# Kernel tuning notes

Hardware: AMD Instinct MI355X
Metric: run time of the kernel (lower is better)

## Reference

```python
import jax, jax.numpy as jnp
import numpy as np

N = 8192          # number of samples (atoms)
D_IN = 256        # in_features (descriptor dim)
D_OUT = 256       # out_features
NUM_TYPE = 64     # number of atom types
INIT_VAL = 0.01


def setup_inputs() -> dict:
    key = jax.random.key(0)
    k1, k2, k3, k4 = jax.random.split(key, 4)
    batch_i = jax.random.randint(k1, (N,), 0, NUM_TYPE)                     # [N] type index per sample
    batch_descriptor = jax.random.normal(k2, (N, D_IN), dtype=jnp.float32)  # [N, D_IN]
    layer1 = INIT_VAL * jax.random.normal(k3, (NUM_TYPE, D_OUT, D_IN), dtype=jnp.float32)
    W = INIT_VAL * jax.random.normal(k4, (D_OUT, D_IN), dtype=jnp.float32)  # linear_adjust.weight
    b = jnp.zeros((D_OUT,), dtype=jnp.float32)                              # linear_adjust.bias (init 0)
    return {"batch_i": batch_i, "batch_descriptor": batch_descriptor,
            "layer1": layer1, "W": W, "b": b}


def reference(batch_i, batch_descriptor, layer1, W, b):
    # Per-sample type-indexed weight gather + batched mat-vec (torch.bmm)
    # layer1[batch_i]: [N, D_OUT, D_IN]; descriptor: [N, D_IN] -> [N, D_OUT]
    gathered = layer1[batch_i]
    out = jnp.einsum('noi,ni->no', gathered, batch_descriptor)
    out = jnp.tanh(out)  # ACT assumed tanh (undefined in snippet)
    # linear_adjust: x @ W.T + b
    adjust = batch_descriptor @ W.T + b
    return out + adjust
```

## Files before the change

kernel.cpp:

```cpp
#include <hip/hip_runtime.h>
#include <cstddef>

#define NUM_TYPE 64
#define DD 256
#define NN 8192
#define GM32 320
#define LSTR 40

typedef __bf16 bf16x8 __attribute__((ext_vector_type(8)));
typedef __bf16 bf16x4 __attribute__((ext_vector_type(4)));
typedef float f32x4 __attribute__((ext_vector_type(4)));

__device__ __forceinline__ bf16x4 cvt4(float4 v) {
  bf16x4 h;
  h[0] = (__bf16)v.x; h[1] = (__bf16)v.y; h[2] = (__bf16)v.z; h[3] = (__bf16)v.w;
  return h;
}

__device__ __forceinline__ float tanh_fast(float x) {
  float xc = fminf(fmaxf(x, -15.f), 15.f);
  float e = __expf(2.f * xc);
  return (e - 1.f) / (e + 1.f);
}

__global__ __launch_bounds__(1024) void build_perm32(
    const int* __restrict__ bi, int* __restrict__ type_off,
    int* __restrict__ perm, int* __restrict__ gtype, int* __restrict__ gfirst) {
  __shared__ int wcnt[16][NUM_TYPE];
  __shared__ int wbase[16][NUM_TYPE];
  __shared__ int cnt[NUM_TYPE];
  __shared__ int tstart[NUM_TYPE];
  __shared__ int gbase[NUM_TYPE];
  __shared__ int totals[2];
  const int tid = threadIdx.x;
  const int w = tid >> 6;
  for (int i = tid; i < 16 * NUM_TYPE; i += 1024) ((int*)wcnt)[i] = 0;
  __syncthreads();
  int myv[8];
#pragma unroll
  for (int rnd = 0; rnd < 8; ++rnd) {
    int v = bi[rnd * 1024 + tid];
    myv[rnd] = v;
    atomicAdd(&wcnt[w][v], 1);
  }
  __syncthreads();
  if (tid < NUM_TYPE) {
    int s = 0;
#pragma unroll
    for (int ww = 0; ww < 16; ++ww) { wbase[ww][tid] = s; s += wcnt[ww][tid]; }
    cnt[tid] = s;
  }
  __syncthreads();
  if (tid == 0) {
    int s = 0, p = 0;
    for (int t = 0; t < NUM_TYPE; ++t) {
      tstart[t] = s; gbase[t] = p;
      s += cnt[t];
      p += (cnt[t] + 31) >> 5;
    }
    totals[0] = s; totals[1] = p;
  }
  __syncthreads();
  if (tid < NUM_TYPE) {
    const int c = cnt[tid];
    const int ngr = (c + 31) >> 5;
    const int g0 = gbase[tid];
    const int s0 = tstart[tid];
    for (int j = 0; j < ngr; ++j) { gtype[g0 + j] = tid; gfirst[g0 + j] = s0 + j * 32; }
    type_off[tid] = s0;
    int b = s0;
#pragma unroll
    for (int ww = 0; ww < 16; ++ww) wbase[ww][tid] += b;
  }
  if (tid == 0) type_off[NUM_TYPE] = totals[0];
  for (int g = totals[1] + tid; g < GM32; g += 1024) gtype[g] = -1;
  __syncthreads();
#pragma unroll
  for (int rnd = 0; rnd < 8; ++rnd) {
    int v = myv[rnd];
    int p = atomicAdd(&wbase[w][v], 1);
    perm[p] = rnd * 1024 + tid;
  }
}

__global__ __launch_bounds__(256) void gemm_tile(
    const float* __restrict__ desc,
    const float* __restrict__ layer1,
    const float* __restrict__ W,
    const float* __restrict__ bias,
    const int* __restrict__ type_off,
    const int* __restrict__ perm,
    const int* __restrict__ gtype,
    const int* __restrict__ gfirst,
    float* __restrict__ out) {
  const int d = blockIdx.x;
  const int l = (d & 7) * 160 + (d >> 3);
  const int g = l >> 2;
  const int cb = l & 3;
  const int t = gtype[g];
  if (t < 0) return;
  const int first = gfirst[g];
  const int limit = type_off[t + 1];

  const int tid = threadIdx.x;
  const int w = tid >> 6;
  const int lane = tid & 63;
  const int l15 = lane & 15;
  const int lg = lane >> 4;
  const int wr = w >> 1;
  const int wc = w & 1;

  __shared__ __bf16 At[2][32][LSTR];
  __shared__ __bf16 Bl[2][64][LSTR];
  __shared__ __bf16 Bw[2][64][LSTR];

  const int srow = tid >> 3;
  const int seg = tid & 7;
  const int ar = first + srow;
  const int sA = (ar < limit) ? perm[ar] : -1;
  const float* aP   = desc + (size_t)(sA < 0 ? 0 : sA) * DD + seg * 4;
  const int gc0 = cb * 64 + srow;
  const float* blP0 = layer1 + ((size_t)t * DD + gc0) * DD + seg * 4;
  const float* blP1 = blP0 + (size_t)32 * DD;
  const float* bwP0 = W + (size_t)gc0 * DD + seg * 4;
  const float* bwP1 = bwP0 + (size_t)32 * DD;

#define STAGE(buf, kb)                                                        \
  {                                                                           \
    float4 va = make_float4(0.f, 0.f, 0.f, 0.f);                              \
    if (sA >= 0) va = *reinterpret_cast<const float4*>(aP + (kb));            \
    *reinterpret_cast<bf16x4*>(&At[buf][srow][seg * 4]) = cvt4(va);           \
    *reinterpret_cast<bf16x4*>(&Bl[buf][srow][seg * 4]) =                     \
        cvt4(*reinterpret_cast<const float4*>(blP0 + (kb)));                  \
    *reinterpret_cast<bf16x4*>(&Bl[buf][srow + 32][seg * 4]) =                \
        cvt4(*reinterpret_cast<const float4*>(blP1 + (kb)));                  \
    *reinterpret_cast<bf16x4*>(&Bw[buf][srow][seg * 4]) =                     \
        cvt4(*reinterpret_cast<const float4*>(bwP0 + (kb)));                  \
    *reinterpret_cast<bf16x4*>(&Bw[buf][srow + 32][seg * 4]) =                \
        cvt4(*reinterpret_cast<const float4*>(bwP1 + (kb)));                  \
  }

  STAGE(0, 0)
  __syncthreads();

  f32x4 accL[2] = {{0.f,0.f,0.f,0.f},{0.f,0.f,0.f,0.f}};
  f32x4 accW[2] = {{0.f,0.f,0.f,0.f},{0.f,0.f,0.f,0.f}};
  int buf = 0;
#pragma unroll
  for (int kc = 0; kc < 8; ++kc) {
    if (kc < 7) STAGE(buf ^ 1, (kc + 1) * 32)
    bf16x8 af = *reinterpret_cast<const bf16x8*>(&At[buf][wr * 16 + l15][lg * 8]);
    bf16x8 b0 = *reinterpret_cast<const bf16x8*>(&Bl[buf][wc * 32 + l15][lg * 8]);
    bf16x8 b1 = *reinterpret_cast<const bf16x8*>(&Bl[buf][wc * 32 + 16 + l15][lg * 8]);
    bf16x8 w0 = *reinterpret_cast<const bf16x8*>(&Bw[buf][wc * 32 + l15][lg * 8]);
    bf16x8 w1 = *reinterpret_cast<const bf16x8*>(&Bw[buf][wc * 32 + 16 + l15][lg * 8]);
    accL[0] = __builtin_amdgcn_mfma_f32_16x16x32_bf16(af, b0, accL[0], 0, 0, 0);
    accL[1] = __builtin_amdgcn_mfma_f32_16x16x32_bf16(af, b1, accL[1], 0, 0, 0);
    accW[0] = __builtin_amdgcn_mfma_f32_16x16x32_bf16(af, w0, accW[0], 0, 0, 0);
    accW[1] = __builtin_amdgcn_mfma_f32_16x16x32_bf16(af, w1, accW[1], 0, 0, 0);
    __syncthreads();
    buf ^= 1;
  }
#undef STAGE

  const int orow = first + wr * 16 + l15;
  const int sOut = (orow < limit) ? perm[orow] : -1;
#pragma unroll
  for (int n = 0; n < 2; ++n) {
    const int col = cb * 64 + wc * 32 + n * 16 + l15;
    const float bv = bias[col];
#pragma unroll
    for (int i = 0; i < 4; ++i) {
      const int sv = __shfl(sOut, lg * 4 + i, 64);
      if (sv >= 0)
        __builtin_nontemporal_store(tanh_fast(accL[n][i]) + accW[n][i] + bv,
                                    out + (size_t)sv * DD + col);
    }
  }
}

extern "C" void kernel_launch(void* const* d_in, const int* in_sizes, int n_in,
                              void* d_out, int out_size, void* d_ws, size_t ws_size,
                              hipStream_t stream) {
  const int* bi       = (const int*)d_in[0];
  const float* desc   = (const float*)d_in[1];
  const float* layer1 = (const float*)d_in[2];
  const float* W      = (const float*)d_in[3];
  const float* bias   = (const float*)d_in[4];
  float* out = (float*)d_out;

  char* ws = (char*)d_ws;
  int* type_off = (int*)(ws);
  int* gtype    = (int*)(ws + 1024);
  int* gfirst   = (int*)(ws + 4096);
  int* perm     = (int*)(ws + 8192);

  hipLaunchKernelGGL(build_perm32, dim3(1), dim3(1024), 0, stream,
                     bi, type_off, perm, gtype, gfirst);
  hipLaunchKernelGGL(gemm_tile, dim3(GM32 * 4), dim3(256), 0, stream,
                     desc, layer1, W, bias, type_off, perm, gtype, gfirst, out);
}
```

Measured before the change: 26.27 us.

## Enlarge GEMM tiles to 128x128 with per-type 128-row groups

Samples are now grouped into 128-row chunks per atom type instead of 32-row chunks. Each 512-thread block computes a 128x128 output tile, with every wave doing 2x4 MFMA fragments for both the layer1 and W products. The aim is to cut how often each type's weight slice and W are re-fetched, and to raise MFMA work per LDS load. The cost is more padding waste, since partially filled groups are larger, and a much smaller grid (256 blocks), which lowers parallelism and latency hiding.

```diff
diff --git a/kernel.cpp b/kernel.cpp
--- a/kernel.cpp
+++ b/kernel.cpp
@@ -4,7 +4,7 @@
 #define NUM_TYPE 64
 #define DD 256
 #define NN 8192
-#define GM32 320
+#define GM128 128
 #define LSTR 40
 
 typedef __bf16 bf16x8 __attribute__((ext_vector_type(8)));
@@ -23,7 +23,7 @@
   return (e - 1.f) / (e + 1.f);
 }
 
-__global__ __launch_bounds__(1024) void build_perm32(
+__global__ __launch_bounds__(1024) void build_perm128(
     const int* __restrict__ bi, int* __restrict__ type_off,
     int* __restrict__ perm, int* __restrict__ gtype, int* __restrict__ gfirst) {
   __shared__ int wcnt[16][NUM_TYPE];
@@ -56,24 +56,23 @@
     for (int t = 0; t < NUM_TYPE; ++t) {
       tstart[t] = s; gbase[t] = p;
       s += cnt[t];
-      p += (cnt[t] + 31) >> 5;
+      p += (cnt[t] + 127) >> 7;
     }
     totals[0] = s; totals[1] = p;
   }
   __syncthreads();
   if (tid < NUM_TYPE) {
     const int c = cnt[tid];
-    const int ngr = (c + 31) >> 5;
+    const int ngr = (c + 127) >> 7;
     const int g0 = gbase[tid];
     const int s0 = tstart[tid];
-    for (int j = 0; j < ngr; ++j) { gtype[g0 + j] = tid; gfirst[g0 + j] = s0 + j * 32; }
+    for (int j = 0; j < ngr; ++j) { gtype[g0 + j] = tid; gfirst[g0 + j] = s0 + j * 128; }
     type_off[tid] = s0;
-    int b = s0;
-#pragma unroll
-    for (int ww = 0; ww < 16; ++ww) wbase[ww][tid] += b;
+#pragma unroll
+    for (int ww = 0; ww < 16; ++ww) wbase[ww][tid] += s0;
   }
   if (tid == 0) type_off[NUM_TYPE] = totals[0];
-  for (int g = totals[1] + tid; g < GM32; g += 1024) gtype[g] = -1;
+  for (int g = totals[1] + tid; g < GM128; g += 1024) gtype[g] = -1;
   __syncthreads();
 #pragma unroll
   for (int rnd = 0; rnd < 8; ++rnd) {
@@ -83,7 +82,7 @@
   }
 }
 
-__global__ __launch_bounds__(256) void gemm_tile(
+__global__ __launch_bounds__(512) void gemm_tile(
     const float* __restrict__ desc,
     const float* __restrict__ layer1,
     const float* __restrict__ W,
@@ -94,9 +93,9 @@
     const int* __restrict__ gfirst,
     float* __restrict__ out) {
   const int d = blockIdx.x;
-  const int l = (d & 7) * 160 + (d >> 3);
-  const int g = l >> 2;
-  const int cb = l & 3;
+  const int l = (d & 7) * 32 + (d >> 3);
+  const int g = l >> 1;
+  const int cb = l & 1;
   const int t = gtype[g];
   if (t < 0) return;
   const int first = gfirst[g];
@@ -110,71 +109,85 @@
   const int wr = w >> 1;
   const int wc = w & 1;
 
-  __shared__ __bf16 At[2][32][LSTR];
-  __shared__ __bf16 Bl[2][64][LSTR];
-  __shared__ __bf16 Bw[2][64][LSTR];
-
-  const int srow = tid >> 3;
-  const int seg = tid & 7;
+  __shared__ __bf16 At[2][128][LSTR];
+  __shared__ __bf16 Bl[2][128][LSTR];
+  __shared__ __bf16 Bw[2][128][LSTR];
+
+  const int srow = tid >> 2;
+  const int fseg = tid & 3;
   const int ar = first + srow;
   const int sA = (ar < limit) ? perm[ar] : -1;
-  const float* aP   = desc + (size_t)(sA < 0 ? 0 : sA) * DD + seg * 4;
-  const int gc0 = cb * 64 + srow;
-  const float* blP0 = layer1 + ((size_t)t * DD + gc0) * DD + seg * 4;
-  const float* blP1 = blP0 + (size_t)32 * DD;
-  const float* bwP0 = W + (size_t)gc0 * DD + seg * 4;
-  const float* bwP1 = bwP0 + (size_t)32 * DD;
+  const float* aP  = desc + (size_t)(sA < 0 ? 0 : sA) * DD + fseg * 8;
+  const int gcol = cb * 128 + srow;
+  const float* blP = layer1 + ((size_t)t * DD + gcol) * DD + fseg * 8;
+  const float* bwP = W + (size_t)gcol * DD + fseg * 8;
 
 #define STAGE(buf, kb)                                                        \
   {                                                                           \
-    float4 va = make_float4(0.f, 0.f, 0.f, 0.f);                              \
-    if (sA >= 0) va = *reinterpret_cast<const float4*>(aP + (kb));            \
-    *reinterpret_cast<bf16x4*>(&At[buf][srow][seg * 4]) = cvt4(va);           \
-    *reinterpret_cast<bf16x4*>(&Bl[buf][srow][seg * 4]) =                     \
-        cvt4(*reinterpret_cast<const float4*>(blP0 + (kb)));                  \
-    *reinterpret_cast<bf16x4*>(&Bl[buf][srow + 32][seg * 4]) =                \
-        cvt4(*reinterpret_cast<const float4*>(blP1 + (kb)));                  \
-    *reinterpret_cast<bf16x4*>(&Bw[buf][srow][seg * 4]) =                     \
-        cvt4(*reinterpret_cast<const float4*>(bwP0 + (kb)));                  \
-    *reinterpret_cast<bf16x4*>(&Bw[buf][srow + 32][seg * 4]) =                \
-        cvt4(*reinterpret_cast<const float4*>(bwP1 + (kb)));                  \
+    float4 a0 = make_float4(0.f,0.f,0.f,0.f), a1 = a0;                        \
+    if (sA >= 0) {                                                            \
+      a0 = *reinterpret_cast<const float4*>(aP + (kb));                       \
+      a1 = *reinterpret_cast<const float4*>(aP + (kb) + 4);                   \
+    }                                                                         \
+    float4 b0 = *reinterpret_cast<const float4*>(blP + (kb));                 \
+    float4 b1 = *reinterpret_cast<const float4*>(blP + (kb) + 4);             \
+    float4 w0 = *reinterpret_cast<const float4*>(bwP + (kb));                 \
+    float4 w1 = *reinterpret_cast<const float4*>(bwP + (kb) + 4);             \
+    *reinterpret_cast<bf16x4*>(&At[buf][srow][fseg * 8])     = cvt4(a0);      \
+    *reinterpret_cast<bf16x4*>(&At[buf][srow][fseg * 8 + 4]) = cvt4(a1);      \
+    *reinterpret_cast<bf16x4*>(&Bl[buf][srow][fseg * 8])     = cvt4(b0);      \
+    *reinterpret_cast<bf16x4*>(&Bl[buf][srow][fseg * 8 + 4]) = cvt4(b1);      \
+    *reinterpret_cast<bf16x4*>(&Bw[buf][srow][fseg * 8])     = cvt4(w0);      \
+    *reinterpret_cast<bf16x4*>(&Bw[buf][srow][fseg * 8 + 4]) = cvt4(w1);      \
   }
 
   STAGE(0, 0)
   __syncthreads();
 
-  f32x4 accL[2] = {{0.f,0.f,0.f,0.f},{0.f,0.f,0.f,0.f}};
-  f32x4 accW[2] = {{0.f,0.f,0.f,0.f},{0.f,0.f,0.f,0.f}};
+  f32x4 accL[2][4] = {};
+  f32x4 accW[2][4] = {};
   int buf = 0;
 #pragma unroll
   for (int kc = 0; kc < 8; ++kc) {
     if (kc < 7) STAGE(buf ^ 1, (kc + 1) * 32)
-    bf16x8 af = *reinterpret_cast<const bf16x8*>(&At[buf][wr * 16 + l15][lg * 8]);
-    bf16x8 b0 = *reinterpret_cast<const bf16x8*>(&Bl[buf][wc * 32 + l15][lg * 8]);
-    bf16x8 b1 = *reinterpret_cast<const bf16x8*>(&Bl[buf][wc * 32 + 16 + l15][lg * 8]);
-    bf16x8 w0 = *reinterpret_cast<const bf16x8*>(&Bw[buf][wc * 32 + l15][lg * 8]);
-    bf16x8 w1 = *reinterpret_cast<const bf16x8*>(&Bw[buf][wc * 32 + 16 + l15][lg * 8]);
-    accL[0] = __builtin_amdgcn_mfma_f32_16x16x32_bf16(af, b0, accL[0], 0, 0, 0);
-    accL[1] = __builtin_amdgcn_mfma_f32_16x16x32_bf16(af, b1, accL[1], 0, 0, 0);
-    accW[0] = __builtin_amdgcn_mfma_f32_16x16x32_bf16(af, w0, accW[0], 0, 0, 0);
-    accW[1] = __builtin_amdgcn_mfma_f32_16x16x32_bf16(af, w1, accW[1], 0, 0, 0);
+    bf16x8 af[2], bl[4], bw[4];
+#pragma unroll
+    for (int m = 0; m < 2; ++m)
+      af[m] = *reinterpret_cast<const bf16x8*>(&At[buf][wr * 32 + m * 16 + l15][lg * 8]);
+#pragma unroll
+    for (int n = 0; n < 4; ++n) {
+      bl[n] = *reinterpret_cast<const bf16x8*>(&Bl[buf][wc * 64 + n * 16 + l15][lg * 8]);
+      bw[n] = *reinterpret_cast<const bf16x8*>(&Bw[buf][wc * 64 + n * 16 + l15][lg * 8]);
+    }
+#pragma unroll
+    for (int m = 0; m < 2; ++m)
+#pragma unroll
+      for (int n = 0; n < 4; ++n) {
+        accL[m][n] = __builtin_amdgcn_mfma_f32_16x16x32_bf16(af[m], bl[n], accL[m][n], 0, 0, 0);
+        accW[m][n] = __builtin_amdgcn_mfma_f32_16x16x32_bf16(af[m], bw[n], accW[m][n], 0, 0, 0);
+      }
     __syncthreads();
     buf ^= 1;
   }
 #undef STAGE
 
-  const int orow = first + wr * 16 + l15;
-  const int sOut = (orow < limit) ? perm[orow] : -1;
-#pragma unroll
-  for (int n = 0; n < 2; ++n) {
-    const int col = cb * 64 + wc * 32 + n * 16 + l15;
-    const float bv = bias[col];
+  float bv[4];
+#pragma unroll
+  for (int n = 0; n < 4; ++n) bv[n] = bias[cb * 128 + wc * 64 + n * 16 + l15];
+#pragma unroll
+  for (int m = 0; m < 2; ++m) {
+    const int orow = first + wr * 32 + m * 16 + l15;
+    const int sOut = (orow < limit) ? perm[orow] : -1;
 #pragma unroll
     for (int i = 0; i < 4; ++i) {
       const int sv = __shfl(sOut, lg * 4 + i, 64);
-      if (sv >= 0)
-        __builtin_nontemporal_store(tanh_fast(accL[n][i]) + accW[n][i] + bv,
-                                    out + (size_t)sv * DD + col);
+      if (sv >= 0) {
+        float* op = out + (size_t)sv * DD + cb * 128 + wc * 64 + l15;
+#pragma unroll
+        for (int n = 0; n < 4; ++n)
+          __builtin_nontemporal_store(tanh_fast(accL[m][n][i]) + accW[m][n][i] + bv[n],
+                                      op + n * 16);
+      }
     }
   }
 }
@@ -195,8 +208,8 @@
   int* gfirst   = (int*)(ws + 4096);
   int* perm     = (int*)(ws + 8192);
 
-  hipLaunchKernelGGL(build_perm32, dim3(1), dim3(1024), 0, stream,
+  hipLaunchKernelGGL(build_perm128, dim3(1), dim3(1024), 0, stream,
                      bi, type_off, perm, gtype, gfirst);
-  hipLaunchKernelGGL(gemm_tile, dim3(GM32 * 4), dim3(256), 0, stream,
+  hipLaunchKernelGGL(gemm_tile, dim3(GM128 * 2), dim3(512), 0, stream,
                      desc, layer1, W, bias, type_off, perm, gtype, gfirst, out);
 }
```

After: 28.20 us. +7.4%, slower.
